# Kernel optimization log

Hardware: AMD Instinct MI355X
Metric: run time of the kernel (lower is better)

## Reference

```python
import jax, jax.numpy as jnp
import numpy as np

B, S, V, D, F, NC = 256, 64, 100000, 64, 10, 10  # batch, seq, vocab, emb_dim, n_feats, n_clusters


def setup_inputs() -> dict:
    key = jax.random.key(0)
    ks = jax.random.split(key, 12)
    ids = jax.random.randint(ks[0], (B, S), 0, V)
    emb_table = jax.random.normal(ks[1], (V, D), dtype=jnp.float32) * 0.02
    comb_w1 = jax.random.normal(ks[2], (2 * D, D), dtype=jnp.float32) / np.sqrt(2 * D)
    comb_b1 = jnp.zeros((D,), jnp.float32)
    comb_w2 = jax.random.normal(ks[3], (D, F), dtype=jnp.float32) / np.sqrt(D)
    comb_b2 = jnp.zeros((F,), jnp.float32)
    freq_w1 = jax.random.normal(ks[4], (D + 1, D), dtype=jnp.float32) / np.sqrt(D + 1)
    freq_b1 = jnp.zeros((D,), jnp.float32)
    freq_w2 = jax.random.normal(ks[5], (D, F), dtype=jnp.float32) / np.sqrt(D)
    freq_b2 = jnp.zeros((F,), jnp.float32)
    cluster_centers = jax.random.normal(ks[6], (NC, D), dtype=jnp.float32)
    cat_freq = jnp.ones((V,), jnp.float32)          # category_frequencies buffer
    total_samples = jnp.array(1.0, jnp.float32)     # total_samples buffer
    return dict(category_ids=ids, emb_table=emb_table,
                comb_w1=comb_w1, comb_b1=comb_b1, comb_w2=comb_w2, comb_b2=comb_b2,
                freq_w1=freq_w1, freq_b1=freq_b1, freq_w2=freq_w2, freq_b2=freq_b2,
                cluster_centers=cluster_centers, cat_freq=cat_freq,
                total_samples=total_samples)


def reference(category_ids, emb_table, comb_w1, comb_b1, comb_w2, comb_b2,
              freq_w1, freq_b1, freq_w2, freq_b2, cluster_centers,
              cat_freq, total_samples):
    emb = emb_table[category_ids]                      # [B,S,D]
    # --- pairwise combination features (vectorized over all i<j pairs) ---
    iu, ju = np.triu_indices(S, 1)                     # P = S*(S-1)/2 pairs
    P = iu.shape[0]
    pairs = jnp.concatenate([emb[:, iu], emb[:, ju]], axis=-1)   # [B,P,2D]
    h = jax.nn.relu(jnp.einsum('bpe,ed->bpd', pairs, comb_w1) + comb_b1)
    combo = jnp.einsum('bpd,df->bpf', h, comb_w2) + comb_b2      # [B,P,F]
    combo_sum = combo.sum(axis=1)                      # [B,F]
    # --- frequency features ---
    freqs = cat_freq[category_ids] / total_samples     # [B,S]
    freq_in = jnp.concatenate([emb, freqs[..., None]], axis=-1)  # [B,S,D+1]
    fh = jax.nn.relu(jnp.einsum('bse,ed->bsd', freq_in, freq_w1) + freq_b1)
    freq_feat = jnp.einsum('bsd,df->bsf', fh, freq_w2) + freq_b2  # [B,S,F]
    # --- cluster assignment features (softmax over -euclidean distances) ---
    d2 = (jnp.sum(emb * emb, axis=-1, keepdims=True)
          + jnp.sum(cluster_centers * cluster_centers, axis=-1)
          - 2.0 * jnp.einsum('bsd,cd->bsc', emb, cluster_centers))
    dist = jnp.sqrt(jnp.maximum(d2, 0.0))              # [B,S,NC]
    cluster_feat = jax.nn.softmax(-dist, axis=-1)      # [B,S,F] (F==NC)
    # --- mean over stacked features: freq + P pair feats (broadcast over seq) + cluster ---
    out = (freq_feat + combo_sum[:, None, :] + cluster_feat) / (P + 2)
    return out
```

## Files before the change

kernel.cpp:

```cpp
#include <hip/hip_runtime.h>
#include <math.h>


typedef _Float16 h2 __attribute__((ext_vector_type(2)));
typedef _Float16 h4 __attribute__((ext_vector_type(4)));
typedef _Float16 h8 __attribute__((ext_vector_type(8)));
union H4u { h4 v; h2 h[2]; };
union H8u { h8 v; h2 h[4]; };

constexpr int BATCH = 256;
constexpr int S = 64, D = 64, F = 10;
constexpr int NPAIR = S * (S - 1) / 2;

constexpr int EMBS = 6144;
constexpr int U2B  = 8192;
constexpr int V2T  = 10240;
constexpr int FHT  = 12352;
constexpr int EMBT = 12352;
constexpr int CF_F = 14528;
constexpr int DI_F = 15168;
constexpr int W2P  = 15808;
constexpr int PART_F = 0;
constexpr int FF_F   = 2048;
constexpr int CS_F   = 2752;

__device__ __forceinline__ h2 pk2(float a, float b) {
#if __has_builtin(__builtin_amdgcn_cvt_pkrtz)
  auto t = __builtin_amdgcn_cvt_pkrtz(a, b);
  return __builtin_bit_cast(h2, t);
#else
  h2 r; r.x = (_Float16)a; r.y = (_Float16)b; return r;
#endif
}

__device__ __forceinline__ float fdot2f(h2 a, h2 b, float c) {
#if __has_builtin(__builtin_amdgcn_fdot2)
  typedef __fp16 q2 __attribute__((ext_vector_type(2)));
  return __builtin_amdgcn_fdot2(__builtin_bit_cast(q2, a),
                                __builtin_bit_cast(q2, b), c, false);
#else
  return c + (float)a.x * (float)b.x + (float)a.y * (float)b.y;
#endif
}

__device__ __forceinline__ h2 hmax2z(h2 a) {
#if __has_builtin(__builtin_elementwise_max)
  h2 z = {(_Float16)0, (_Float16)0};
  return __builtin_elementwise_max(a, z);
#else
  h2 r;
  r.x = a.x > (_Float16)0 ? a.x : (_Float16)0;
  r.y = a.y > (_Float16)0 ? a.y : (_Float16)0;
  return r;
#endif
}

__device__ __forceinline__ float lane_up1(float v) {
#if __has_builtin(__builtin_amdgcn_update_dpp)
  int r = __builtin_amdgcn_update_dpp(0, __float_as_int(v), 0xF5, 0xF, 0xF, false);
  return __int_as_float(r);
#else
  return __shfl_down(v, 1, 64);
#endif
}

__global__ __launch_bounds__(1024, 4)
void cat_enc_kernel(const int*   __restrict__ ids,
                    const float* __restrict__ emb_table,
                    const float* __restrict__ comb_w1,
                    const float* __restrict__ comb_b1,
                    const float* __restrict__ comb_w2,
                    const float* __restrict__ comb_b2,
                    const float* __restrict__ freq_w1,
                    const float* __restrict__ freq_b1,
                    const float* __restrict__ freq_w2,
                    const float* __restrict__ freq_b2,
                    const float* __restrict__ centers,
                    const float* __restrict__ cat_freq,
                    const float* __restrict__ total_samples,
                    float*       __restrict__ out)
{
  __shared__ __align__(16) unsigned int ldsu[16128];
  h2*    ldsH = (h2*)ldsu;
  float* ldsf = (float*)ldsu;
  const int tid = threadIdx.x;
  const int b = blockIdx.x, bBase = b * S;

  {
    int s = tid >> 4, q = tid & 15;
    int id = ids[bBase + s];
    float4 e4 = *(const float4*)(emb_table + (size_t)id * D + q * 4);
    h2 p0 = pk2(e4.x, e4.y), p1 = pk2(e4.z, e4.w);
    ldsH[EMBS + s * 32 + q * 2]     = p0;
    ldsH[EMBS + s * 32 + q * 2 + 1] = p1;
    ldsH[EMBT + (q * 2) * 64 + s]     = p0;
    ldsH[EMBT + (q * 2 + 1) * 64 + s] = p1;

    {
      const int k4 = tid >> 6, dd = tid & 63;
      const float* s0p = comb_w1 + (k4 * 4) * D + dd;
      const float* s1p = s0p + D * D;
      const float* s2p = freq_w1 + (k4 * 4) * D + dd;
      h4* dst = (h4*)ldsu;
      H4u u0; u0.h[0] = pk2(s0p[0], s0p[D]); u0.h[1] = pk2(s0p[2 * D], s0p[3 * D]);
      H4u u1; u1.h[0] = pk2(s1p[0], s1p[D]); u1.h[1] = pk2(s1p[2 * D], s1p[3 * D]);
      H4u u2; u2.h[0] = pk2(s2p[0], s2p[D]); u2.h[1] = pk2(s2p[2 * D], s2p[3 * D]);
      dst[2 * tid]     = u0.v;
      dst[2 * tid + 1] = u1.v;
      dst[2048 + tid]  = u2.v;
    }
    if (tid < 320) {
      int f = tid >> 5, d2 = tid & 31;
      ldsH[W2P + tid] = pk2(freq_w2[(2 * d2) * F + f], freq_w2[(2 * d2 + 1) * F + f]);
    }
  }
  __syncthreads();

  {
    int wv = __builtin_amdgcn_readfirstlane((int)(tid >> 6));
    int lane = tid & 63;
    if (wv < 10) {
      const float* crow = centers + wv * D;
      float acc = 0.f;
#pragma unroll 8
      for (int k2 = 0; k2 < 32; ++k2) {
        h2 e2 = ldsH[EMBT + k2 * 64 + lane];
        float t0 = (float)e2.x - crow[2 * k2];
        float t1 = (float)e2.y - crow[2 * k2 + 1];
        acc = fmaf(t0, t0, fmaf(t1, t1, acc));
      }
      ldsf[DI_F + lane * 10 + wv] = sqrtf(acc);
    }
  }
  __syncthreads();

  {
    const int d  = tid & 63;
    const int wv = __builtin_amdgcn_readfirstlane((int)(tid >> 6));
    const int s0 = wv * 4;
    const float invT = 1.0f / total_samples[0];
    int idv[4];
#pragma unroll
    for (int si = 0; si < 4; ++si)
      idv[si] = __builtin_amdgcn_readfirstlane(ids[bBase + s0 + si]);
    const float b1d = comb_b1[d], fb1d = freq_b1[d], fw1L = freq_w1[D * D + d];
    float aU[4], aV[4], aF[4];
#pragma unroll
    for (int si = 0; si < 4; ++si) {
      aU[si] = b1d; aV[si] = 0.f;
      aF[si] = fmaf(cat_freq[idv[si]] * invT, fw1L, fb1d);
    }
    const h8* WUVp = (const h8*)ldsu;
    const h4* WFp  = (const h4*)(ldsu + 4096);
#pragma unroll 2
    for (int k8 = 0; k8 < 8; ++k8) {
      const int k4a = 2 * k8, k4b = 2 * k8 + 1;
      H8u wa; wa.v = WUVp[k4a * 64 + d];
      H8u wb; wb.v = WUVp[k4b * 64 + d];
      H4u fa; fa.v = WFp[k4a * 64 + d];
      H4u fb; fb.v = WFp[k4b * 64 + d];
#pragma unroll
      for (int si = 0; si < 4; ++si) {
        H8u e; e.v = *(const h8*)&ldsH[EMBS + (s0 + si) * 32 + k8 * 4];
        aU[si] = fdot2f(e.h[0], wa.h[0], aU[si]);
        aU[si] = fdot2f(e.h[1], wa.h[1], aU[si]);
        aV[si] = fdot2f(e.h[0], wa.h[2], aV[si]);
        aV[si] = fdot2f(e.h[1], wa.h[3], aV[si]);
        aF[si] = fdot2f(e.h[0], fa.h[0], aF[si]);
        aF[si] = fdot2f(e.h[1], fa.h[1], aF[si]);
        aU[si] = fdot2f(e.h[2], wb.h[0], aU[si]);
        aU[si] = fdot2f(e.h[3], wb.h[1], aU[si]);
        aV[si] = fdot2f(e.h[2], wb.h[2], aV[si]);
        aV[si] = fdot2f(e.h[3], wb.h[3], aV[si]);
        aF[si] = fdot2f(e.h[2], fb.h[0], aF[si]);
        aF[si] = fdot2f(e.h[3], fb.h[1], aF[si]);
      }
    }
    const bool evenl = ((d & 1) == 0);
    const int d2 = d >> 1;
#pragma unroll
    for (int si = 0; si < 4; ++si) {
      float un = lane_up1(aU[si]);
      float vn = lane_up1(aV[si]);
      float fh = fmaxf(aF[si], 0.f);
      float fn = lane_up1(fh);
      if (evenl) {
        int srow = s0 + si;
        ldsH[U2B + srow * 32 + d2] = pk2(aU[si], un);
        ldsH[V2T + d2 * 66 + srow] = pk2(aV[si], vn);
        ldsH[FHT + srow * 34 + d2] = pk2(fh, fn);
      }
    }
  }
  __syncthreads();

  {
    if (tid < 640) {
      int s = tid & 63;
      int f = __builtin_amdgcn_readfirstlane((int)(tid >> 6));
      float acc = freq_b2[f];
      const h8* wrow = (const h8*)&ldsH[W2P + f * 32];
#pragma unroll
      for (int d8 = 0; d8 < 4; ++d8) {
        H8u wf; wf.v = wrow[d8];
        H4u f0; f0.v = *(const h4*)&ldsH[FHT + s * 34 + d8 * 4];
        H4u f1; f1.v = *(const h4*)&ldsH[FHT + s * 34 + d8 * 4 + 2];
        acc = fdot2f(f0.h[0], wf.h[0], acc);
        acc = fdot2f(f0.h[1], wf.h[1], acc);
        acc = fdot2f(f1.h[0], wf.h[2], acc);
        acc = fdot2f(f1.h[1], wf.h[3], acc);
      }
      ldsf[FF_F + s * 10 + f] = acc;
    } else if (tid < 704) {
      int s = tid - 640;
      float dv[10], dmin = 1e30f;
#pragma unroll
      for (int c = 0; c < 10; ++c) { dv[c] = ldsf[DI_F + s * 10 + c]; dmin = fminf(dmin, dv[c]); }
      float p[10], sum = 0.f;
#pragma unroll
      for (int c = 0; c < 10; ++c) { p[c] = expf(dmin - dv[c]); sum += p[c]; }
      float rs = 1.0f / sum;
#pragma unroll
      for (int c = 0; c < 10; ++c) ldsf[CF_F + s * 10 + c] = p[c] * rs;
    }
  }

  {
    const int dg = tid & 31, g = tid >> 5;
    h2 u2a = ldsH[U2B + g * 32 + dg];
    h2 u2b = ldsH[U2B + (63 - g) * 32 + dg];
    h2 za = {(_Float16)0, (_Float16)0};
    h2 acA0 = za, acA1 = za, accb = za;
    const int jsplit = 64 - g;
    int j = g + 1;
    if (j & 1) {
      h2 v2 = ldsH[V2T + dg * 66 + j];
      acA0 = acA0 + hmax2z(u2a + v2);
      ++j;
    }
#pragma unroll 4
    for (; j < 64; j += 2) {
      H4u v; v.v = *(const h4*)&ldsH[V2T + dg * 66 + j];
      acA0 = acA0 + hmax2z(u2a + v.h[0]);
      acA1 = acA1 + hmax2z(u2a + v.h[1]);
      if (j + 1 >= jsplit) {
        if (j >= jsplit) accb = accb + hmax2z(u2b + v.h[0]);
        accb = accb + hmax2z(u2b + v.h[1]);
      }
    }
    h2 at = acA0 + acA1 + accb;
    ldsf[PART_F + g * 64 + 2 * dg]     = (float)at.x;
    ldsf[PART_F + g * 64 + 2 * dg + 1] = (float)at.y;
  }
  __syncthreads();

  if (tid < 64) {
    float h = 0.f;
#pragma unroll
    for (int g2 = 0; g2 < 32; ++g2) h += ldsf[PART_F + g2 * 64 + tid];
    float csv = 0.f;
#pragma unroll
    for (int f = 0; f < 10; ++f) {
      float p = h * comb_w2[tid * F + f];
#pragma unroll
      for (int off = 1; off < 64; off <<= 1) p += __shfl_xor(p, off, 64);
      if (tid == f) csv = p;
    }
    if (tid < 10) ldsf[CS_F + tid] = fmaf(comb_b2[tid], (float)NPAIR, csv);
  }
  __syncthreads();

  if (tid < 640) {
    int f = tid % 10;
    float val = (ldsf[FF_F + tid] + ldsf[CS_F + f] + ldsf[CF_F + tid])
              * (1.0f / (float)(NPAIR + 2));
    out[(size_t)b * 640 + tid] = val;
  }
}

extern "C" void kernel_launch(void* const* d_in, const int* in_sizes, int n_in,
                              void* d_out, int out_size, void* d_ws, size_t ws_size,
                              hipStream_t stream) {
  (void)in_sizes; (void)n_in; (void)d_ws; (void)ws_size; (void)out_size;
  const int*   ids        = (const int*)  d_in[0];
  const float* emb_table  = (const float*)d_in[1];
  const float* comb_w1    = (const float*)d_in[2];
  const float* comb_b1    = (const float*)d_in[3];
  const float* comb_w2    = (const float*)d_in[4];
  const float* comb_b2    = (const float*)d_in[5];
  const float* freq_w1    = (const float*)d_in[6];
  const float* freq_b1    = (const float*)d_in[7];
  const float* freq_w2    = (const float*)d_in[8];
  const float* freq_b2    = (const float*)d_in[9];
  const float* centers    = (const float*)d_in[10];
  const float* cat_freq   = (const float*)d_in[11];
  const float* total_samp = (const float*)d_in[12];
  float* out = (float*)d_out;

  hipLaunchKernelGGL(cat_enc_kernel, dim3(BATCH), dim3(1024), 0, stream,
                     ids, emb_table, comb_w1, comb_b1, comb_w2, comb_b2,
                     freq_w1, freq_b1, freq_w2, freq_b2, centers, cat_freq,
                     total_samp, out);
}
```

Before: 105.1 us.

## Run cluster distances concurrently with layer-1 matmul and drop transposed embedding copy

Merges the cluster-distance phase and the first-layer projection phase into one barrier-delimited stage. Waves 0-7 compute U/V/F hidden vectors for 8 sequence rows each, and waves 8-15 compute the ten center distances from the row-major embedding copy held in registers. This removes one __syncthreads and the transposed EMBT copy. The embedding row stride is padded to 36 halves, and the softmax output reuses the distance buffer in place to shrink LDS. The cost is more accumulator registers per matmul wave and a less balanced split of work across waves.

```diff
diff --git a/kernel.cpp b/kernel.cpp
--- a/kernel.cpp
+++ b/kernel.cpp
@@ -13,13 +13,11 @@
 constexpr int NPAIR = S * (S - 1) / 2;
 
 constexpr int EMBS = 6144;
-constexpr int U2B  = 8192;
-constexpr int V2T  = 10240;
-constexpr int FHT  = 12352;
-constexpr int EMBT = 12352;
-constexpr int CF_F = 14528;
-constexpr int DI_F = 15168;
-constexpr int W2P  = 15808;
+constexpr int U2B  = 8448;
+constexpr int V2T  = 10496;
+constexpr int FHT  = 12608;
+constexpr int DI_F = 14784;
+constexpr int W2P  = 15424;
 constexpr int PART_F = 0;
 constexpr int FF_F   = 2048;
 constexpr int CS_F   = 2752;
@@ -80,7 +78,7 @@
                     const float* __restrict__ total_samples,
                     float*       __restrict__ out)
 {
-  __shared__ __align__(16) unsigned int ldsu[16128];
+  __shared__ __align__(16) unsigned int ldsu[15744];
   h2*    ldsH = (h2*)ldsu;
   float* ldsf = (float*)ldsu;
   const int tid = threadIdx.x;
@@ -90,11 +88,8 @@
     int s = tid >> 4, q = tid & 15;
     int id = ids[bBase + s];
     float4 e4 = *(const float4*)(emb_table + (size_t)id * D + q * 4);
-    h2 p0 = pk2(e4.x, e4.y), p1 = pk2(e4.z, e4.w);
-    ldsH[EMBS + s * 32 + q * 2]     = p0;
-    ldsH[EMBS + s * 32 + q * 2 + 1] = p1;
-    ldsH[EMBT + (q * 2) * 64 + s]     = p0;
-    ldsH[EMBT + (q * 2 + 1) * 64 + s] = p1;
+    H4u ep; ep.h[0] = pk2(e4.x, e4.y); ep.h[1] = pk2(e4.z, e4.w);
+    *(h4*)&ldsH[EMBS + s * 36 + q * 2] = ep.v;
 
     {
       const int k4 = tid >> 6, dd = tid & 63;
@@ -117,78 +112,80 @@
   __syncthreads();
 
   {
-    int wv = __builtin_amdgcn_readfirstlane((int)(tid >> 6));
-    int lane = tid & 63;
-    if (wv < 10) {
-      const float* crow = centers + wv * D;
-      float acc = 0.f;
-#pragma unroll 8
-      for (int k2 = 0; k2 < 32; ++k2) {
-        h2 e2 = ldsH[EMBT + k2 * 64 + lane];
-        float t0 = (float)e2.x - crow[2 * k2];
-        float t1 = (float)e2.y - crow[2 * k2 + 1];
-        acc = fmaf(t0, t0, fmaf(t1, t1, acc));
-      }
-      ldsf[DI_F + lane * 10 + wv] = sqrtf(acc);
-    }
-  }
-  __syncthreads();
-
-  {
-    const int d  = tid & 63;
-    const int wv = __builtin_amdgcn_readfirstlane((int)(tid >> 6));
-    const int s0 = wv * 4;
-    const float invT = 1.0f / total_samples[0];
-    int idv[4];
-#pragma unroll
-    for (int si = 0; si < 4; ++si)
-      idv[si] = __builtin_amdgcn_readfirstlane(ids[bBase + s0 + si]);
-    const float b1d = comb_b1[d], fb1d = freq_b1[d], fw1L = freq_w1[D * D + d];
-    float aU[4], aV[4], aF[4];
-#pragma unroll
-    for (int si = 0; si < 4; ++si) {
-      aU[si] = b1d; aV[si] = 0.f;
-      aF[si] = fmaf(cat_freq[idv[si]] * invT, fw1L, fb1d);
-    }
-    const h8* WUVp = (const h8*)ldsu;
-    const h4* WFp  = (const h4*)(ldsu + 4096);
+    const int wv   = __builtin_amdgcn_readfirstlane((int)(tid >> 6));
+    const int lane = tid & 63;
+    if (wv < 8) {
+      const int d  = lane;
+      const int s0 = wv * 8;
+      const float invT = 1.0f / total_samples[0];
+      const float b1d = comb_b1[d], fb1d = freq_b1[d], fw1L = freq_w1[D * D + d];
+      float aU[8], aV[8], aF[8];
+#pragma unroll
+      for (int si = 0; si < 8; ++si) {
+        int idv = __builtin_amdgcn_readfirstlane(ids[bBase + s0 + si]);
+        aU[si] = b1d; aV[si] = 0.f;
+        aF[si] = fmaf(cat_freq[idv] * invT, fw1L, fb1d);
+      }
+      const h8* WUVp = (const h8*)ldsu;
+      const h4* WFp  = (const h4*)(ldsu + 4096);
 #pragma unroll 2
-    for (int k8 = 0; k8 < 8; ++k8) {
-      const int k4a = 2 * k8, k4b = 2 * k8 + 1;
-      H8u wa; wa.v = WUVp[k4a * 64 + d];
-      H8u wb; wb.v = WUVp[k4b * 64 + d];
-      H4u fa; fa.v = WFp[k4a * 64 + d];
-      H4u fb; fb.v = WFp[k4b * 64 + d];
-#pragma unroll
-      for (int si = 0; si < 4; ++si) {
-        H8u e; e.v = *(const h8*)&ldsH[EMBS + (s0 + si) * 32 + k8 * 4];
-        aU[si] = fdot2f(e.h[0], wa.h[0], aU[si]);
-        aU[si] = fdot2f(e.h[1], wa.h[1], aU[si]);
-        aV[si] = fdot2f(e.h[0], wa.h[2], aV[si]);
-        aV[si] = fdot2f(e.h[1], wa.h[3], aV[si]);
-        aF[si] = fdot2f(e.h[0], fa.h[0], aF[si]);
-        aF[si] = fdot2f(e.h[1], fa.h[1], aF[si]);
-        aU[si] = fdot2f(e.h[2], wb.h[0], aU[si]);
-        aU[si] = fdot2f(e.h[3], wb.h[1], aU[si]);
-        aV[si] = fdot2f(e.h[2], wb.h[2], aV[si]);
-        aV[si] = fdot2f(e.h[3], wb.h[3], aV[si]);
-        aF[si] = fdot2f(e.h[2], fb.h[0], aF[si]);
-        aF[si] = fdot2f(e.h[3], fb.h[1], aF[si]);
-      }
-    }
-    const bool evenl = ((d & 1) == 0);
-    const int d2 = d >> 1;
-#pragma unroll
-    for (int si = 0; si < 4; ++si) {
-      float un = lane_up1(aU[si]);
-      float vn = lane_up1(aV[si]);
-      float fh = fmaxf(aF[si], 0.f);
-      float fn = lane_up1(fh);
-      if (evenl) {
-        int srow = s0 + si;
-        ldsH[U2B + srow * 32 + d2] = pk2(aU[si], un);
-        ldsH[V2T + d2 * 66 + srow] = pk2(aV[si], vn);
-        ldsH[FHT + srow * 34 + d2] = pk2(fh, fn);
+      for (int k8 = 0; k8 < 8; ++k8) {
+        H8u wa; wa.v = WUVp[(2 * k8) * 64 + d];
+        H8u wb; wb.v = WUVp[(2 * k8 + 1) * 64 + d];
+        H4u fa; fa.v = WFp[(2 * k8) * 64 + d];
+        H4u fb; fb.v = WFp[(2 * k8 + 1) * 64 + d];
+#pragma unroll
+        for (int si = 0; si < 8; ++si) {
+          H8u e; e.v = *(const h8*)&ldsH[EMBS + (s0 + si) * 36 + k8 * 4];
+          aU[si] = fdot2f(e.h[0], wa.h[0], aU[si]);
+          aU[si] = fdot2f(e.h[1], wa.h[1], aU[si]);
+          aV[si] = fdot2f(e.h[0], wa.h[2], aV[si]);
+          aV[si] = fdot2f(e.h[1], wa.h[3], aV[si]);
+          aF[si] = fdot2f(e.h[0], fa.h[0], aF[si]);
+          aF[si] = fdot2f(e.h[1], fa.h[1], aF[si]);
+          aU[si] = fdot2f(e.h[2], wb.h[0], aU[si]);
+          aU[si] = fdot2f(e.h[3], wb.h[1], aU[si]);
+          aV[si] = fdot2f(e.h[2], wb.h[2], aV[si]);
+          aV[si] = fdot2f(e.h[3], wb.h[3], aV[si]);
+          aF[si] = fdot2f(e.h[2], fb.h[0], aF[si]);
+          aF[si] = fdot2f(e.h[3], fb.h[1], aF[si]);
+        }
+      }
+      const bool evenl = ((d & 1) == 0);
+      const int d2 = d >> 1;
+#pragma unroll
+      for (int si = 0; si < 8; ++si) {
+        float un = lane_up1(aU[si]);
+        float vn = lane_up1(aV[si]);
+        float fh = fmaxf(aF[si], 0.f);
+        float fn = lane_up1(fh);
+        if (evenl) {
+          int srow = s0 + si;
+          ldsH[U2B + srow * 32 + d2] = pk2(aU[si], un);
+          ldsH[V2T + d2 * 66 + srow] = pk2(aV[si], vn);
+          ldsH[FHT + srow * 34 + d2] = pk2(fh, fn);
+        }
+      }
+    } else {
+      const int s = lane;
+      H8u er[8];
+#pragma unroll
+      for (int k8 = 0; k8 < 8; ++k8)
+        er[k8].v = *(const h8*)&ldsH[EMBS + s * 36 + k8 * 4];
+      for (int cc = wv - 8; cc < 10; cc += 8) {
+        const float* crow = centers + cc * D;
+        float acc = 0.f;
+#pragma unroll
+        for (int k8 = 0; k8 < 8; ++k8) {
+#pragma unroll
+          for (int t = 0; t < 4; ++t) {
+            const int k2 = k8 * 4 + t;
+            float t0 = (float)er[k8].h[t].x - crow[2 * k2];
+            float t1 = (float)er[k8].h[t].y - crow[2 * k2 + 1];
+            acc = fmaf(t0, t0, fmaf(t1, t1, acc));
+          }
+        }
+        ldsf[DI_F + s * 10 + cc] = sqrtf(acc);
       }
     }
   }
@@ -221,7 +218,7 @@
       for (int c = 0; c < 10; ++c) { p[c] = expf(dmin - dv[c]); sum += p[c]; }
       float rs = 1.0f / sum;
 #pragma unroll
-      for (int c = 0; c < 10; ++c) ldsf[CF_F + s * 10 + c] = p[c] * rs;
+      for (int c = 0; c < 10; ++c) ldsf[DI_F + s * 10 + c] = p[c] * rs;
     }
   }
 
@@ -272,7 +269,7 @@
 
   if (tid < 640) {
     int f = tid % 10;
-    float val = (ldsf[FF_F + tid] + ldsf[CS_F + f] + ldsf[CF_F + tid])
+    float val = (ldsf[FF_F + tid] + ldsf[CS_F + f] + ldsf[DI_F + tid])
               * (1.0f / (float)(NPAIR + 2));
     out[(size_t)b * 640 + tid] = val;
   }
```

Measured after the change: 109.4 us. +4.1%, slower.
